# Kernel optimization log

Measured on AMD Instinct MI355X. Metric: run time of the kernel, lower is better.

The kernel has to match this reference:

```python
import jax, jax.numpy as jnp
import numpy as np

B, D, T = 16384, 1024, 128  # batch, embed_dim, num_degradation_types
V, L = 4, 3                 # variants per sample, degradations per variant


def setup_inputs() -> dict:
    key = jax.random.key(0)
    k1, k2, k3, k4 = jax.random.split(key, 4)
    clean_embeddings = jax.random.normal(k1, (B, D), dtype=jnp.float32)
    W = jax.random.normal(k2, (T, D), dtype=jnp.float32) * (1.0 / np.sqrt(D))
    b = jnp.zeros((T,), dtype=jnp.float32)
    deg_indices = jax.random.randint(k3, (B, V, L), 0, T, dtype=jnp.int32)
    deg_mask = jax.random.randint(k4, (B, V, L), 0, 2, dtype=jnp.int32)
    return {"clean_embeddings": clean_embeddings, "W": W, "b": b,
            "deg_indices": deg_indices, "deg_mask": deg_mask}


def reference(clean_embeddings, W, b, deg_indices, deg_mask):
    # Linear + softmax: [B, T]
    logits = jnp.einsum("bd,td->bt", clean_embeddings, W) + b
    probs = jax.nn.softmax(logits, axis=-1)
    # Gather probs at each (batch, label) pair: [B, V*L] -> [B, V, L]
    flat_idx = deg_indices.reshape(B, V * L)
    gathered = jnp.take_along_axis(probs, flat_idx, axis=1).reshape(B, V, L)
    # Masked sum over all labels of a sample, divided by max(num_variants, 1)=V
    per_sample = (gathered * deg_mask.astype(probs.dtype)).sum(axis=(1, 2)) / V
    return per_sample.sum() / B
```

## Files before the change

kernel.cpp:

```cpp
#include <hip/hip_runtime.h>

#define B_SIZE 16384
#define D_DIM  1024
#define T_DIM  128
#define VLn    12
#define BM     32
#define BK     64
#define NCHUNK (D_DIM / BK)
#define GRID   (B_SIZE / BM)
#define SL_STRIDE 132

typedef _Float16 half8  __attribute__((ext_vector_type(8)));
typedef __fp16   fp16x2 __attribute__((ext_vector_type(2)));
typedef float    f32x4  __attribute__((ext_vector_type(4)));

union Pack16 { fp16x2 h[4]; uint4 u; };
union BReg   { uint4 u; half8 h; };

__device__ __forceinline__ uint4 pack8(float4 v0, float4 v1) {
    Pack16 un;
    un.h[0] = __builtin_amdgcn_cvt_pkrtz(v0.x, v0.y);
    un.h[1] = __builtin_amdgcn_cvt_pkrtz(v0.z, v0.w);
    un.h[2] = __builtin_amdgcn_cvt_pkrtz(v1.x, v1.y);
    un.h[3] = __builtin_amdgcn_cvt_pkrtz(v1.z, v1.w);
    return un.u;
}

__global__ __launch_bounds__(256)
void conv_w(const float* __restrict__ W, uint4* __restrict__ Wf) {
    const int j    = blockIdx.x * 256 + threadIdx.x;
    const int kc   = j >> 10;
    const int r    = j & 1023;
    const int g    = r >> 6;
    const int lane = r & 63;
    const int ks = g >> 3, CT = g & 7;
    const int n = CT * 16 + (lane & 15);
    const int k = kc * 64 + ks * 32 + ((lane >> 4) << 3);
    const float* src = W + (size_t)n * D_DIM + k;
    const float4 v0 = *(const float4*)src;
    const float4 v1 = *(const float4*)(src + 4);
    Wf[j] = pack8(v0, v1);
}

__global__ __launch_bounds__(256, 2)
void qloss_kernel(const float* __restrict__ emb,
                  const uint4* __restrict__ Wf,
                  const float* __restrict__ bias,
                  const int*   __restrict__ didx,
                  const int*   __restrict__ dmsk,
                  float*       __restrict__ out)
{
    __shared__ __align__(16) unsigned char smem[16928];
    float* sL   = (float*)smem;
    float* sRed = (float*)(smem + 16896);

    const int t    = threadIdx.x;
    const int w    = t >> 6;
    const int lane = t & 63;
    const int m15  = lane & 15;
    const int quad = lane >> 4;
    const int r0   = blockIdx.x * BM;

    const int sg   = t >> 6, sl = t & 63;
    const int srow = (sg >> 1) * 16 + (sl & 15);
    const int skk  = (sg & 1) * 32 + ((sl >> 4) << 3);
    const float* aBase = emb + (size_t)(r0 + srow) * D_DIM + skk;

    const uint4* wBase = Wf + (size_t)(2 * w) * 64 + lane;

    f32x4 acc[2][2];
#pragma unroll
    for (int mt = 0; mt < 2; ++mt)
#pragma unroll
        for (int ct = 0; ct < 2; ++ct) acc[mt][ct] = (f32x4){0.f, 0.f, 0.f, 0.f};

    BReg bcur[4], bnx1[4], bnx2[4];
    float4 an0, an1, af0, af1;
    {
        const float4 v0 = *(const float4*)(aBase);
        const float4 v1 = *(const float4*)(aBase + 4);
        an0 = *(const float4*)(aBase + 64);
        an1 = *(const float4*)(aBase + 68);
#pragma unroll
        for (int ks = 0; ks < 2; ++ks)
#pragma unroll
            for (int j = 0; j < 2; ++j) {
                bcur[ks * 2 + j].u = wBase[(size_t)(ks * 8 + j) * 64];
                bnx1[ks * 2 + j].u = wBase[(size_t)1 * 1024 + (ks * 8 + j) * 64];
            }
        *(uint4*)(smem + t * 16) = pack8(v0, v1);
    }
    __syncthreads();

#pragma unroll
    for (int kc = 0; kc < NCHUNK; ++kc) {
        unsigned char* sAc = smem + (kc & 1) * 4096;
        unsigned char* sAn = smem + ((kc & 1) ^ 1) * 4096;

        if (kc + 2 < NCHUNK) {
            af0 = *(const float4*)(aBase + (kc + 2) * 64);
            af1 = *(const float4*)(aBase + (kc + 2) * 64 + 4);
#pragma unroll
            for (int ks = 0; ks < 2; ++ks)
#pragma unroll
                for (int j = 0; j < 2; ++j)
                    bnx2[ks * 2 + j].u =
                        wBase[(size_t)(kc + 2) * 1024 + (ks * 8 + j) * 64];
        }

#pragma unroll
        for (int ks = 0; ks < 2; ++ks) {
            const half8 a0 = *(const half8*)(sAc + ((0 * 2 + ks) * 64 + lane) * 16);
            const half8 a1 = *(const half8*)(sAc + ((1 * 2 + ks) * 64 + lane) * 16);
            acc[0][0] = __builtin_amdgcn_mfma_f32_16x16x32_f16(a0, bcur[ks * 2 + 0].h, acc[0][0], 0, 0, 0);
            acc[0][1] = __builtin_amdgcn_mfma_f32_16x16x32_f16(a0, bcur[ks * 2 + 1].h, acc[0][1], 0, 0, 0);
            acc[1][0] = __builtin_amdgcn_mfma_f32_16x16x32_f16(a1, bcur[ks * 2 + 0].h, acc[1][0], 0, 0, 0);
            acc[1][1] = __builtin_amdgcn_mfma_f32_16x16x32_f16(a1, bcur[ks * 2 + 1].h, acc[1][1], 0, 0, 0);
        }

        if (kc + 1 < NCHUNK)
            *(uint4*)(sAn + t * 16) = pack8(an0, an1);
        __syncthreads();

        an0 = af0; an1 = af1;
#pragma unroll
        for (int q = 0; q < 4; ++q) { bcur[q] = bnx1[q]; bnx1[q] = bnx2[q]; }
    }

    const int CT0 = w * 2;
    const float b0v = bias[CT0 * 16 + m15];
    const float b1v = bias[(CT0 + 1) * 16 + m15];
#pragma unroll
    for (int mt = 0; mt < 2; ++mt)
#pragma unroll
        for (int i = 0; i < 4; ++i) {
            const int row = mt * 16 + quad * 4 + i;
            sL[row * SL_STRIDE + CT0 * 16 + m15]       = acc[mt][0][i] + b0v;
            sL[row * SL_STRIDE + (CT0 + 1) * 16 + m15] = acc[mt][1][i] + b1v;
        }
    __syncthreads();

    {
        const int row = t >> 3, s = t & 7;
        float* base = &sL[row * SL_STRIDE + s * 16];
        float v[16];
#pragma unroll
        for (int j = 0; j < 4; ++j) *(float4*)&v[j * 4] = *(const float4*)(base + j * 4);
        float m = -1e30f;
#pragma unroll
        for (int j = 0; j < 16; ++j) m = fmaxf(m, v[j]);
#pragma unroll
        for (int off = 1; off < 8; off <<= 1) m = fmaxf(m, __shfl_xor(m, off));
        float ssum = 0.f;
#pragma unroll
        for (int j = 0; j < 16; ++j) { v[j] = __expf(v[j] - m); ssum += v[j]; }
#pragma unroll
        for (int off = 1; off < 8; off <<= 1) ssum += __shfl_xor(ssum, off);
        const float inv = 1.0f / ssum;
#pragma unroll
        for (int j = 0; j < 16; ++j) v[j] *= inv;
#pragma unroll
        for (int j = 0; j < 4; ++j) *(float4*)(base + j * 4) = *(const float4*)&v[j * 4];
    }
    __syncthreads();

    float p = 0.f;
#pragma unroll
    for (int i = t; i < BM * VLn; i += 256) {
        const int gi  = r0 * VLn + i;
        const int row = i / VLn;
        const int idx = didx[gi];
        const int mk  = dmsk[gi];
        p += mk ? sL[row * SL_STRIDE + idx] : 0.f;
    }
#pragma unroll
    for (int off = 1; off < 64; off <<= 1) p += __shfl_xor(p, off);
    if (lane == 0) sRed[w] = p;
    __syncthreads();
    if (t == 0)
        atomicAdd(out, (sRed[0] + sRed[1] + sRed[2] + sRed[3]) * (1.0f / 65536.0f));
}

extern "C" void kernel_launch(void* const* d_in, const int* in_sizes, int n_in,
                              void* d_out, int out_size, void* d_ws, size_t ws_size,
                              hipStream_t stream) {
    const float* emb  = (const float*)d_in[0];
    const float* W    = (const float*)d_in[1];
    const float* bias = (const float*)d_in[2];
    const int*   didx = (const int*)d_in[3];
    const int*   dmsk = (const int*)d_in[4];
    float* out = (float*)d_out;

    uint4* Wf = (uint4*)d_ws;

    hipMemsetAsync(out, 0, sizeof(float), stream);
    conv_w<<<64, 256, 0, stream>>>(W, Wf);
    qloss_kernel<<<GRID, 256, 0, stream>>>(emb, Wf, bias, didx, dmsk, out);
}
```

Measured before the change: 114.6 us.

## Load A fragments directly from global per wave, dropping shared staging and barriers

Each wave now loads its own fp32 embedding fragments for all 32 rows straight from global memory into registers and converts them to fp16 right before the MFMAs. This removes the LDS double buffer and the per-chunk __syncthreads. In exchange, every one of the four waves reads the full 32x1024 A tile, so global/L2 read traffic for embeddings rises fourfold. Prefetch depth also drops from two chunks to one, which could expose more memory latency.

```diff
diff --git a/kernel.cpp b/kernel.cpp
--- a/kernel.cpp
+++ b/kernel.cpp
@@ -5,8 +5,7 @@
 #define T_DIM  128
 #define VLn    12
 #define BM     32
-#define BK     64
-#define NCHUNK (D_DIM / BK)
+#define NCHUNK 16
 #define GRID   (B_SIZE / BM)
 #define SL_STRIDE 132
 
@@ -14,10 +13,18 @@
 typedef __fp16   fp16x2 __attribute__((ext_vector_type(2)));
 typedef float    f32x4  __attribute__((ext_vector_type(4)));
 
-union Pack16 { fp16x2 h[4]; uint4 u; };
+union Pack16 { fp16x2 h[4]; uint4 u; half8 v; };
 union BReg   { uint4 u; half8 h; };
 
-__device__ __forceinline__ uint4 pack8(float4 v0, float4 v1) {
+__device__ __forceinline__ half8 pack8h(float4 v0, float4 v1) {
+    Pack16 un;
+    un.h[0] = __builtin_amdgcn_cvt_pkrtz(v0.x, v0.y);
+    un.h[1] = __builtin_amdgcn_cvt_pkrtz(v0.z, v0.w);
+    un.h[2] = __builtin_amdgcn_cvt_pkrtz(v1.x, v1.y);
+    un.h[3] = __builtin_amdgcn_cvt_pkrtz(v1.z, v1.w);
+    return un.v;
+}
+__device__ __forceinline__ uint4 pack8u(float4 v0, float4 v1) {
     Pack16 un;
     un.h[0] = __builtin_amdgcn_cvt_pkrtz(v0.x, v0.y);
     un.h[1] = __builtin_amdgcn_cvt_pkrtz(v0.z, v0.w);
@@ -39,7 +46,7 @@
     const float* src = W + (size_t)n * D_DIM + k;
     const float4 v0 = *(const float4*)src;
     const float4 v1 = *(const float4*)(src + 4);
-    Wf[j] = pack8(v0, v1);
+    Wf[j] = pack8u(v0, v1);
 }
 
 __global__ __launch_bounds__(256, 2)
@@ -50,7 +57,7 @@
                   const int*   __restrict__ dmsk,
                   float*       __restrict__ out)
 {
-    __shared__ __align__(16) unsigned char smem[16928];
+    __shared__ __align__(16) unsigned char smem[16912];
     float* sL   = (float*)smem;
     float* sRed = (float*)(smem + 16896);
 
@@ -61,12 +68,9 @@
     const int quad = lane >> 4;
     const int r0   = blockIdx.x * BM;
 
-    const int sg   = t >> 6, sl = t & 63;
-    const int srow = (sg >> 1) * 16 + (sl & 15);
-    const int skk  = (sg & 1) * 32 + ((sl >> 4) << 3);
-    const float* aBase = emb + (size_t)(r0 + srow) * D_DIM + skk;
-
-    const uint4* wBase = Wf + (size_t)(2 * w) * 64 + lane;
+    const float* aR0 = emb + (size_t)(r0 + m15) * D_DIM + quad * 8;
+    const float* aR1 = aR0 + 16 * D_DIM;
+    const uint4* bP  = Wf + (size_t)(2 * w) * 64 + lane;
 
     f32x4 acc[2][2];
 #pragma unroll
@@ -74,57 +78,56 @@
 #pragma unroll
         for (int ct = 0; ct < 2; ++ct) acc[mt][ct] = (f32x4){0.f, 0.f, 0.f, 0.f};
 
-    BReg bcur[4], bnx1[4], bnx2[4];
-    float4 an0, an1, af0, af1;
-    {
-        const float4 v0 = *(const float4*)(aBase);
-        const float4 v1 = *(const float4*)(aBase + 4);
-        an0 = *(const float4*)(aBase + 64);
-        an1 = *(const float4*)(aBase + 68);
-#pragma unroll
-        for (int ks = 0; ks < 2; ++ks)
-#pragma unroll
-            for (int j = 0; j < 2; ++j) {
-                bcur[ks * 2 + j].u = wBase[(size_t)(ks * 8 + j) * 64];
-                bnx1[ks * 2 + j].u = wBase[(size_t)1 * 1024 + (ks * 8 + j) * 64];
-            }
-        *(uint4*)(smem + t * 16) = pack8(v0, v1);
-    }
-    __syncthreads();
+    float4 ac[8], an[8];
+    BReg   bc[4], bn[4];
+
+#pragma unroll
+    for (int mt = 0; mt < 2; ++mt)
+#pragma unroll
+        for (int ks = 0; ks < 2; ++ks) {
+            const float* p = (mt ? aR1 : aR0) + ks * 32;
+            ac[mt * 4 + ks * 2 + 0] = *(const float4*)(p);
+            ac[mt * 4 + ks * 2 + 1] = *(const float4*)(p + 4);
+        }
+#pragma unroll
+    for (int ks = 0; ks < 2; ++ks)
+#pragma unroll
+        for (int j = 0; j < 2; ++j)
+            bc[ks * 2 + j].u = bP[(size_t)(ks * 8 + j) * 64];
 
 #pragma unroll
     for (int kc = 0; kc < NCHUNK; ++kc) {
-        unsigned char* sAc = smem + (kc & 1) * 4096;
-        unsigned char* sAn = smem + ((kc & 1) ^ 1) * 4096;
-
-        if (kc + 2 < NCHUNK) {
-            af0 = *(const float4*)(aBase + (kc + 2) * 64);
-            af1 = *(const float4*)(aBase + (kc + 2) * 64 + 4);
+        if (kc + 1 < NCHUNK) {
+            const int ko = (kc + 1) * 64;
+#pragma unroll
+            for (int mt = 0; mt < 2; ++mt)
+#pragma unroll
+                for (int ks = 0; ks < 2; ++ks) {
+                    const float* p = (mt ? aR1 : aR0) + ko + ks * 32;
+                    an[mt * 4 + ks * 2 + 0] = *(const float4*)(p);
+                    an[mt * 4 + ks * 2 + 1] = *(const float4*)(p + 4);
+                }
 #pragma unroll
             for (int ks = 0; ks < 2; ++ks)
 #pragma unroll
                 for (int j = 0; j < 2; ++j)
-                    bnx2[ks * 2 + j].u =
-                        wBase[(size_t)(kc + 2) * 1024 + (ks * 8 + j) * 64];
+                    bn[ks * 2 + j].u = bP[(size_t)(kc + 1) * 1024 + (ks * 8 + j) * 64];
         }
 
 #pragma unroll
         for (int ks = 0; ks < 2; ++ks) {
-            const half8 a0 = *(const half8*)(sAc + ((0 * 2 + ks) * 64 + lane) * 16);
-            const half8 a1 = *(const half8*)(sAc + ((1 * 2 + ks) * 64 + lane) * 16);
-            acc[0][0] = __builtin_amdgcn_mfma_f32_16x16x32_f16(a0, bcur[ks * 2 + 0].h, acc[0][0], 0, 0, 0);
-            acc[0][1] = __builtin_amdgcn_mfma_f32_16x16x32_f16(a0, bcur[ks * 2 + 1].h, acc[0][1], 0, 0, 0);
-            acc[1][0] = __builtin_amdgcn_mfma_f32_16x16x32_f16(a1, bcur[ks * 2 + 0].h, acc[1][0], 0, 0, 0);
-            acc[1][1] = __builtin_amdgcn_mfma_f32_16x16x32_f16(a1, bcur[ks * 2 + 1].h, acc[1][1], 0, 0, 0);
-        }
-
-        if (kc + 1 < NCHUNK)
-            *(uint4*)(sAn + t * 16) = pack8(an0, an1);
-        __syncthreads();
-
-        an0 = af0; an1 = af1;
-#pragma unroll
-        for (int q = 0; q < 4; ++q) { bcur[q] = bnx1[q]; bnx1[q] = bnx2[q]; }
+            const half8 a0 = pack8h(ac[0 + ks * 2], ac[1 + ks * 2]);
+            const half8 a1 = pack8h(ac[4 + ks * 2], ac[5 + ks * 2]);
+            acc[0][0] = __builtin_amdgcn_mfma_f32_16x16x32_f16(a0, bc[ks * 2 + 0].h, acc[0][0], 0, 0, 0);
+            acc[0][1] = __builtin_amdgcn_mfma_f32_16x16x32_f16(a0, bc[ks * 2 + 1].h, acc[0][1], 0, 0, 0);
+            acc[1][0] = __builtin_amdgcn_mfma_f32_16x16x32_f16(a1, bc[ks * 2 + 0].h, acc[1][0], 0, 0, 0);
+            acc[1][1] = __builtin_amdgcn_mfma_f32_16x16x32_f16(a1, bc[ks * 2 + 1].h, acc[1][1], 0, 0, 0);
+        }
+
+#pragma unroll
+        for (int q = 0; q < 8; ++q) ac[q] = an[q];
+#pragma unroll
+        for (int q = 0; q < 4; ++q) bc[q] = bn[q];
     }
 
     const int CT0 = w * 2;
```

New measurement: 138.0 us. +20.5%, slower.
